# Optimization experiments

Measured on AMD Instinct MI355X. Metric: run time of the kernel, lower is better.

Reference implementation:

```python
import jax, jax.numpy as jnp
import numpy as np

N = 100000   # nodes
C = 128      # in_channels
K = 32       # n_super_nodes
B = 64       # graphs (num segments)


def setup_inputs() -> dict:
    key = jax.random.key(0)
    k_x, k_b, k_w1, k_b1, k_w2, k_b2 = jax.random.split(key, 6)
    x = jax.random.normal(k_x, (N, C), dtype=jnp.float32)
    batch = jnp.sort(jax.random.randint(k_b, (N,), 0, B))
    # assign_mlp params: Linear(C,C) -> ReLU -> Linear(C,K); stored as [in,out]
    W1 = jax.random.normal(k_w1, (C, C), dtype=jnp.float32) / np.sqrt(C)
    b1 = jax.random.normal(k_b1, (C,), dtype=jnp.float32) * 0.01
    W2 = jax.random.normal(k_w2, (C, K), dtype=jnp.float32) / np.sqrt(C)
    b2 = jax.random.normal(k_b2, (K,), dtype=jnp.float32) * 0.01
    return {"x": x, "batch": batch, "W1": W1, "b1": b1, "W2": W2, "b2": b2}


def reference(x, batch, W1, b1, W2, b2):
    # assignment logits: MLP over node features
    h = jax.nn.relu(x @ W1 + b1)          # [N, C]
    s = jax.nn.softmax(h @ W2 + b2, axis=-1)  # [N, K]
    # outer product per node, then scatter-sum by graph id
    x_expanded = x[:, None, :] * s[:, :, None]  # [N, K, C]
    out = jax.ops.segment_sum(x_expanded, batch, num_segments=B)  # [B, K, C]
    return (out, s)
```

## Files before the change

### kernel.cpp

```cpp
#include <hip/hip_runtime.h>
#include <hip/hip_bf16.h>

#define NN 100000
#define CC 128
#define KK 32
#define BB 64
#define CH 4
#define NCHUNK (NN / 32)

typedef __bf16 bf16x8 __attribute__((ext_vector_type(8)));
typedef float  f32x4  __attribute__((ext_vector_type(4)));

__device__ __forceinline__ unsigned short f2bf(float v) {
    union { __bf16 h; unsigned short s; } u;
    u.h = (__bf16)v;
    return u.s;
}
__device__ __forceinline__ float bf2f(unsigned short h) {
    union { unsigned u; float f; } a; a.u = ((unsigned)h) << 16;
    return a.f;
}
__device__ __forceinline__ void unpack_hilo(uint4 a, uint4 b,
                                            bf16x8& hi8, bf16x8& lo8) {
    union { unsigned u[4]; bf16x8 v; } H, L;
    H.u[0] = __builtin_amdgcn_perm(a.y, a.x, 0x05040100u);
    H.u[1] = __builtin_amdgcn_perm(a.w, a.z, 0x05040100u);
    H.u[2] = __builtin_amdgcn_perm(b.y, b.x, 0x05040100u);
    H.u[3] = __builtin_amdgcn_perm(b.w, b.z, 0x05040100u);
    L.u[0] = __builtin_amdgcn_perm(a.y, a.x, 0x07060302u);
    L.u[1] = __builtin_amdgcn_perm(a.w, a.z, 0x07060302u);
    L.u[2] = __builtin_amdgcn_perm(b.y, b.x, 0x07060302u);
    L.u[3] = __builtin_amdgcn_perm(b.w, b.z, 0x07060302u);
    hi8 = H.v; lo8 = L.v;
}

__device__ __forceinline__ void atomAddF(float* p, float v) {
#if defined(__gfx950__) || defined(__gfx942__) || defined(__gfx90a__)
    unsafeAtomicAdd(p, v);
#else
    atomicAdd(p, v);
#endif
}

__global__ __launch_bounds__(256) void hp_prep(const float* __restrict__ W1,
                                               const float* __restrict__ W2,
                                               unsigned short* __restrict__ w1f,
                                               unsigned short* __restrict__ w2f,
                                               float* __restrict__ out_zero) {
    const int t = blockIdx.x * 256 + threadIdx.x;
    {
        const int idx  = t;
        const int j    = idx & 7;
        const int lane = (idx >> 3) & 63;
        const int nt   = (idx >> 9) & 7;
        const int kt   = idx >> 12;
        const int k = kt * 32 + (lane >> 4) * 8 + j;
        const int n = nt * 16 + (lane & 15);
        const float w = W1[k * CC + n];
        const unsigned short h = f2bf(w);
        w1f[idx]         = h;
        w1f[16384 + idx] = f2bf(w - bf2f(h));
    }
    if (t < 4096) {
        const int idx  = t;
        const int j    = idx & 7;
        const int lane = (idx >> 3) & 63;
        const int nt   = (idx >> 9) & 1;
        const int kt   = idx >> 10;
        const int k = kt * 32 + (lane >> 4) * 8 + j;
        const int n = nt * 16 + (lane & 15);
        const float w = W2[k * KK + n];
        const unsigned short h = f2bf(w);
        w2f[idx]        = h;
        w2f[4096 + idx] = f2bf(w - bf2f(h));
    }
    const float4 z = make_float4(0.f, 0.f, 0.f, 0.f);
    for (int i = t; i < BB * KK * CC / 4; i += 16384)
        *(float4*)(out_zero + (size_t)i * 4) = z;
}

__global__ __launch_bounds__(256, 3) void hp_fused(
    const float* __restrict__ x,
    const unsigned short* __restrict__ w1f,
    const unsigned short* __restrict__ w2f,
    const float* __restrict__ b1,
    const float* __restrict__ b2,
    const int* __restrict__ batch,
    float* __restrict__ s_out,
    float* __restrict__ out)
{
    __shared__ __align__(16) char uni[16896];
    __shared__ __align__(16) unsigned short xbL[8 * 64 * 8];
    __shared__ float lgT[32][36];
    __shared__ float redm[4][32];
    __shared__ float reds[4][32];

    unsigned short* xa   = (unsigned short*)uni;
    unsigned int*   hs16 = (unsigned int*)uni;

    const int t    = threadIdx.x;
    const int wave = __builtin_amdgcn_readfirstlane(t >> 6);
    const int lane = t & 63;

    const int pmt   = wave & 1;
    const int chalf = wave >> 1;
    const int nrow  = (lane >> 4) * 8;

    f32x4 pacc[4];
    #pragma unroll
    for (int i = 0; i < 4; ++i) pacc[i] = (f32x4){0.f, 0.f, 0.f, 0.f};

    int cg = __builtin_amdgcn_readfirstlane(batch[blockIdx.x * (CH * 32)]);

    auto flush = [&](int g) {
        float* op = out + (size_t)g * KK * CC;
        #pragma unroll
        for (int i = 0; i < 4; ++i) {
            const int c = (chalf * 4 + i) * 16 + (lane & 15);
            #pragma unroll
            for (int r = 0; r < 4; ++r) {
                const int k = pmt * 16 + (lane >> 4) * 4 + r;
                atomAddF(op + k * CC + c, pacc[i][r]);
            }
            pacc[i] = (f32x4){0.f, 0.f, 0.f, 0.f};
        }
    };

    #pragma unroll 1
    for (int ch = 0; ch < CH; ++ch) {
        const int chunk = blockIdx.x * CH + ch;
        if (chunk >= NCHUNK) break;
        const int base = chunk * 32;

        __syncthreads();

        #pragma unroll
        for (int mt = 0; mt < 2; ++mt) {
            const int q  = mt * 4 + wave;
            const int n  = base + mt * 16 + (lane & 15);
            const int ck = wave * 32 + (lane >> 4) * 8;
            const float4 va = *(const float4*)(x + (size_t)n * CC + ck);
            const float4 vb = *(const float4*)(x + (size_t)n * CC + ck + 4);
            const float v[8] = {va.x, va.y, va.z, va.w, vb.x, vb.y, vb.z, vb.w};
            union { unsigned short s[8]; uint4 u; } H, L;
            #pragma unroll
            for (int j = 0; j < 8; ++j) {
                H.s[j] = f2bf(v[j]);
                L.s[j] = f2bf(v[j] - bf2f(H.s[j]));
            }
            unsigned short* d0 = xa + (q * 64 + lane) * 8;
            *(uint4*)(d0)        = H.u;
            *(uint4*)(d0 + 4096) = L.u;
        }

        #pragma unroll
        for (int cc = 0; cc < 2; ++cc) {
            const int ct = wave * 2 + cc;
            const int c  = ct * 16 + (lane & 15);
            const int nb = base + nrow;
            union { unsigned short s[8]; uint4 u; } Hb;
            #pragma unroll
            for (int j = 0; j < 8; ++j)
                Hb.s[j] = f2bf(x[(size_t)(nb + j) * CC + c]);
            *(uint4*)(xbL + ((size_t)ct * 64 + lane) * 8) = Hb.u;
        }
        __syncthreads();

        f32x4 acc[2][2];
        #pragma unroll
        for (int mt = 0; mt < 2; ++mt)
            #pragma unroll
            for (int nl = 0; nl < 2; ++nl)
                acc[mt][nl] = (f32x4){0.f, 0.f, 0.f, 0.f};

        #pragma unroll
        for (int kt = 0; kt < 4; ++kt) {
            bf16x8 ah[2], al[2];
            #pragma unroll
            for (int mt = 0; mt < 2; ++mt) {
                ah[mt] = *(const bf16x8*)(xa + ((mt * 4 + kt) * 64 + lane) * 8);
                al[mt] = *(const bf16x8*)(xa + 4096 + ((mt * 4 + kt) * 64 + lane) * 8);
            }
            #pragma unroll
            for (int nl = 0; nl < 2; ++nl) {
                const int nt = 2 * wave + nl;
                const bf16x8 wh = *(const bf16x8*)(w1f + ((kt * 8 + nt) * 64 + lane) * 8);
                const bf16x8 wl = *(const bf16x8*)(w1f + 16384 + ((kt * 8 + nt) * 64 + lane) * 8);
                #pragma unroll
                for (int mt = 0; mt < 2; ++mt) {
                    acc[mt][nl] = __builtin_amdgcn_mfma_f32_16x16x32_bf16(ah[mt], wh, acc[mt][nl], 0, 0, 0);
                    acc[mt][nl] = __builtin_amdgcn_mfma_f32_16x16x32_bf16(al[mt], wh, acc[mt][nl], 0, 0, 0);
                    acc[mt][nl] = __builtin_amdgcn_mfma_f32_16x16x32_bf16(ah[mt], wl, acc[mt][nl], 0, 0, 0);
                }
            }
        }
        __syncthreads();

        #pragma unroll
        for (int nl = 0; nl < 2; ++nl) {
            const int c = (2 * wave + nl) * 16 + (lane & 15);
            const float bv = b1[c];
            #pragma unroll
            for (int mt = 0; mt < 2; ++mt)
                #pragma unroll
                for (int r = 0; r < 4; ++r) {
                    const int node = mt * 16 + (lane >> 4) * 4 + r;
                    const float h = fmaxf(acc[mt][nl][r] + bv, 0.f);
                    const unsigned short hi = f2bf(h);
                    const unsigned short lo = f2bf(h - bf2f(hi));
                    hs16[node * 132 + c] = (unsigned)hi | ((unsigned)lo << 16);
                }
        }
        __syncthreads();

        {
            const int mt2 = wave & 1, nt2 = wave >> 1;
            f32x4 dacc = (f32x4){0.f, 0.f, 0.f, 0.f};
            #pragma unroll
            for (int kt = 0; kt < 4; ++kt) {
                const unsigned* hp = hs16 + (mt2 * 16 + (lane & 15)) * 132
                                          + kt * 32 + (lane >> 4) * 8;
                const uint4 u0 = *(const uint4*)hp;
                const uint4 u1 = *(const uint4*)(hp + 4);
                bf16x8 ah, al;
                unpack_hilo(u0, u1, ah, al);
                const bf16x8 wh = *(const bf16x8*)(w2f + ((kt * 2 + nt2) * 64 + lane) * 8);
                const bf16x8 wl = *(const bf16x8*)(w2f + 4096 + ((kt * 2 + nt2) * 64 + lane) * 8);
                dacc = __builtin_amdgcn_mfma_f32_16x16x32_bf16(ah, wh, dacc, 0, 0, 0);
                dacc = __builtin_amdgcn_mfma_f32_16x16x32_bf16(al, wh, dacc, 0, 0, 0);
                dacc = __builtin_amdgcn_mfma_f32_16x16x32_bf16(ah, wl, dacc, 0, 0, 0);
            }
            const int kcol = nt2 * 16 + (lane & 15);
            #pragma unroll
            for (int r = 0; r < 4; ++r) {
                const int node = mt2 * 16 + (lane >> 4) * 4 + r;
                lgT[node][kcol] = dacc[r];
            }
        }
        __syncthreads();

        {
            const int node = lane & 31;
            const int koff = ((lane >> 5) << 4) + wave * 4;
            const float4 bv2 = *(const float4*)(b2 + koff);
            const float4 lv  = *(const float4*)&lgT[node][koff];
            float lg[4] = {lv.x + bv2.x, lv.y + bv2.y, lv.z + bv2.z, lv.w + bv2.w};

            float m = fmaxf(fmaxf(lg[0], lg[1]), fmaxf(lg[2], lg[3]));
            m = fmaxf(m, __shfl_xor(m, 32));
            if (lane < 32) redm[wave][lane] = m;
            __syncthreads();
            const float M = fmaxf(fmaxf(redm[0][node], redm[1][node]),
                                  fmaxf(redm[2][node], redm[3][node]));
            const float e0 = __expf(lg[0] - M);
            const float e1 = __expf(lg[1] - M);
            const float e2 = __expf(lg[2] - M);
            const float e3 = __expf(lg[3] - M);
            float sp = (e0 + e1) + (e2 + e3);
            sp += __shfl_xor(sp, 32);
            if (lane < 32) reds[wave][lane] = sp;
            __syncthreads();
            const float S = (reds[0][node] + reds[1][node]) + (reds[2][node] + reds[3][node]);
            const float inv = 1.f / S;
            const float4 s4 = make_float4(e0 * inv, e1 * inv, e2 * inv, e3 * inv);
            *(float4*)(s_out + (size_t)(base + node) * KK + koff) = s4;
            *(float4*)&lgT[node][koff] = s4;
        }
        __syncthreads();

        {
            union { unsigned short s[8]; bf16x8 v; } A;
            const int kA = pmt * 16 + (lane & 15);
            #pragma unroll
            for (int j = 0; j < 8; ++j)
                A.s[j] = f2bf(lgT[nrow + j][kA]);
            bf16x8 Bv[4];
            #pragma unroll
            for (int i = 0; i < 4; ++i)
                Bv[i] = *(const bf16x8*)(xbL + ((size_t)(chalf * 4 + i) * 64 + lane) * 8);

            const int gl0 = __builtin_amdgcn_readfirstlane(batch[base]);
            const int gh  = __builtin_amdgcn_readfirstlane(batch[base + 31]);

            if (gl0 == cg && gh == cg) {
                #pragma unroll
                for (int i = 0; i < 4; ++i)
                    pacc[i] = __builtin_amdgcn_mfma_f32_16x16x32_bf16(A.v, Bv[i], pacc[i], 0, 0, 0);
            } else {
                int bt[8];
                #pragma unroll
                for (int j = 0; j < 8; ++j) bt[j] = batch[base + nrow + j];
                while (cg < gh) {
                    union { unsigned short s[8]; bf16x8 v; } Am;
                    #pragma unroll
                    for (int j = 0; j < 8; ++j)
                        Am.s[j] = (bt[j] == cg) ? A.s[j] : (unsigned short)0;
                    #pragma unroll
                    for (int i = 0; i < 4; ++i)
                        pacc[i] = __builtin_amdgcn_mfma_f32_16x16x32_bf16(Am.v, Bv[i], pacc[i], 0, 0, 0);
                    flush(cg);
                    ++cg;
                }
                union { unsigned short s[8]; bf16x8 v; } Am;
                #pragma unroll
                for (int j = 0; j < 8; ++j)
                    Am.s[j] = (bt[j] == cg) ? A.s[j] : (unsigned short)0;
                #pragma unroll
                for (int i = 0; i < 4; ++i)
                    pacc[i] = __builtin_amdgcn_mfma_f32_16x16x32_bf16(Am.v, Bv[i], pacc[i], 0, 0, 0);
            }
        }
    }

    flush(cg);
}

extern "C" void kernel_launch(void* const* d_in, const int* in_sizes, int n_in,
                              void* d_out, int out_size, void* d_ws, size_t ws_size,
                              hipStream_t stream) {
    const float* x     = (const float*)d_in[0];
    const int*   batch = (const int*)d_in[1];
    const float* W1    = (const float*)d_in[2];
    const float* b1    = (const float*)d_in[3];
    const float* W2    = (const float*)d_in[4];
    const float* b2    = (const float*)d_in[5];

    float* out = (float*)d_out;
    float* s   = out + (size_t)BB * KK * CC;

    char* ws = (char*)d_ws;
    unsigned short* w1f = (unsigned short*)ws;
    unsigned short* w2f = (unsigned short*)(ws + 65536);

    hp_prep<<<64, 256, 0, stream>>>(W1, W2, w1f, w2f, out);
    const int nblk = (NCHUNK + CH - 1) / CH;
    hp_fused<<<nblk, 256, 0, stream>>>(x, w1f, w2f, b1, b2, batch, s, out);
}
```

Baseline: 132.9 us.

## Fuse logits softmax into MFMA waves and overlap xbL staging with idle waves

Waves 0-1 now compute both 16-column logit tiles and run the softmax in registers with intra-row shuffles. This removes the lgT round-trip, the cross-wave redm/reds reductions and several block barriers. Waves 2-3 stage the bf16 transposed x tile for the pooling MFMA in parallel, and the loop-head barrier is dropped. Bias loads are hoisted out of the loop and launch bounds go from 3 to 4 blocks per CU, which may raise register pressure or cause spills. The s_out stores become scalar strided instead of float4, and the removed loop-top barrier may risk an xbL reuse hazard across chunks.

After: 149.5 us. +12.5%, slower.

```diff
diff --git a/kernel.cpp b/kernel.cpp
--- a/kernel.cpp
+++ b/kernel.cpp
@@ -79,7 +79,7 @@
         *(float4*)(out_zero + (size_t)i * 4) = z;
 }
 
-__global__ __launch_bounds__(256, 3) void hp_fused(
+__global__ __launch_bounds__(256, 4) void hp_fused(
     const float* __restrict__ x,
     const unsigned short* __restrict__ w1f,
     const unsigned short* __restrict__ w2f,
@@ -92,8 +92,6 @@
     __shared__ __align__(16) char uni[16896];
     __shared__ __align__(16) unsigned short xbL[8 * 64 * 8];
     __shared__ float lgT[32][36];
-    __shared__ float redm[4][32];
-    __shared__ float reds[4][32];
 
     unsigned short* xa   = (unsigned short*)uni;
     unsigned int*   hs16 = (unsigned int*)uni;
@@ -105,6 +103,11 @@
     const int pmt   = wave & 1;
     const int chalf = wave >> 1;
     const int nrow  = (lane >> 4) * 8;
+
+    const float bv_epi0 = b1[(2 * wave + 0) * 16 + (lane & 15)];
+    const float bv_epi1 = b1[(2 * wave + 1) * 16 + (lane & 15)];
+    const float b2lo = b2[lane & 15];
+    const float b2hi = b2[16 + (lane & 15)];
 
     f32x4 pacc[4];
     #pragma unroll
@@ -131,8 +134,6 @@
         const int chunk = blockIdx.x * CH + ch;
         if (chunk >= NCHUNK) break;
         const int base = chunk * 32;
-
-        __syncthreads();
 
         #pragma unroll
         for (int mt = 0; mt < 2; ++mt) {
@@ -152,18 +153,6 @@
             *(uint4*)(d0)        = H.u;
             *(uint4*)(d0 + 4096) = L.u;
         }
-
-        #pragma unroll
-        for (int cc = 0; cc < 2; ++cc) {
-            const int ct = wave * 2 + cc;
-            const int c  = ct * 16 + (lane & 15);
-            const int nb = base + nrow;
-            union { unsigned short s[8]; uint4 u; } Hb;
-            #pragma unroll
-            for (int j = 0; j < 8; ++j)
-                Hb.s[j] = f2bf(x[(size_t)(nb + j) * CC + c]);
-            *(uint4*)(xbL + ((size_t)ct * 64 + lane) * 8) = Hb.u;
-        }
         __syncthreads();
 
         f32x4 acc[2][2];
@@ -198,8 +187,8 @@
 
         #pragma unroll
         for (int nl = 0; nl < 2; ++nl) {
+            const float bv = nl ? bv_epi1 : bv_epi0;
             const int c = (2 * wave + nl) * 16 + (lane & 15);
-            const float bv = b1[c];
             #pragma unroll
             for (int mt = 0; mt < 2; ++mt)
                 #pragma unroll
@@ -213,9 +202,11 @@
         }
         __syncthreads();
 
-        {
-            const int mt2 = wave & 1, nt2 = wave >> 1;
-            f32x4 dacc = (f32x4){0.f, 0.f, 0.f, 0.f};
+        if (wave < 2) {
+            const int mt2 = wave;
+            f32x4 dacc[2];
+            dacc[0] = (f32x4){0.f, 0.f, 0.f, 0.f};
+            dacc[1] = (f32x4){0.f, 0.f, 0.f, 0.f};
             #pragma unroll
             for (int kt = 0; kt < 4; ++kt) {
                 const unsigned* hp = hs16 + (mt2 * 16 + (lane & 15)) * 132
@@ -224,47 +215,62 @@
                 const uint4 u1 = *(const uint4*)(hp + 4);
                 bf16x8 ah, al;
                 unpack_hilo(u0, u1, ah, al);
-                const bf16x8 wh = *(const bf16x8*)(w2f + ((kt * 2 + nt2) * 64 + lane) * 8);
-                const bf16x8 wl = *(const bf16x8*)(w2f + 4096 + ((kt * 2 + nt2) * 64 + lane) * 8);
-                dacc = __builtin_amdgcn_mfma_f32_16x16x32_bf16(ah, wh, dacc, 0, 0, 0);
-                dacc = __builtin_amdgcn_mfma_f32_16x16x32_bf16(al, wh, dacc, 0, 0, 0);
-                dacc = __builtin_amdgcn_mfma_f32_16x16x32_bf16(ah, wl, dacc, 0, 0, 0);
-            }
-            const int kcol = nt2 * 16 + (lane & 15);
+                #pragma unroll
+                for (int nt2 = 0; nt2 < 2; ++nt2) {
+                    const bf16x8 wh = *(const bf16x8*)(w2f + ((kt * 2 + nt2) * 64 + lane) * 8);
+                    const bf16x8 wl = *(const bf16x8*)(w2f + 4096 + ((kt * 2 + nt2) * 64 + lane) * 8);
+                    dacc[nt2] = __builtin_amdgcn_mfma_f32_16x16x32_bf16(ah, wh, dacc[nt2], 0, 0, 0);
+                    dacc[nt2] = __builtin_amdgcn_mfma_f32_16x16x32_bf16(al, wh, dacc[nt2], 0, 0, 0);
+                    dacc[nt2] = __builtin_amdgcn_mfma_f32_16x16x32_bf16(ah, wl, dacc[nt2], 0, 0, 0);
+                }
+            }
+            float lg0[4], lg1[4], m[4];
             #pragma unroll
             for (int r = 0; r < 4; ++r) {
+                lg0[r] = dacc[0][r] + b2lo;
+                lg1[r] = dacc[1][r] + b2hi;
+                m[r] = fmaxf(lg0[r], lg1[r]);
+            }
+            #pragma unroll
+            for (int msk = 1; msk < 16; msk <<= 1)
+                #pragma unroll
+                for (int r = 0; r < 4; ++r)
+                    m[r] = fmaxf(m[r], __shfl_xor(m[r], msk));
+            float e0[4], e1[4], sm[4];
+            #pragma unroll
+            for (int r = 0; r < 4; ++r) {
+                e0[r] = __expf(lg0[r] - m[r]);
+                e1[r] = __expf(lg1[r] - m[r]);
+                sm[r] = e0[r] + e1[r];
+            }
+            #pragma unroll
+            for (int msk = 1; msk < 16; msk <<= 1)
+                #pragma unroll
+                for (int r = 0; r < 4; ++r)
+                    sm[r] += __shfl_xor(sm[r], msk);
+            #pragma unroll
+            for (int r = 0; r < 4; ++r) {
+                const float inv = 1.f / sm[r];
+                e0[r] *= inv;
+                e1[r] *= inv;
                 const int node = mt2 * 16 + (lane >> 4) * 4 + r;
-                lgT[node][kcol] = dacc[r];
-            }
-        }
-        __syncthreads();
-
-        {
-            const int node = lane & 31;
-            const int koff = ((lane >> 5) << 4) + wave * 4;
-            const float4 bv2 = *(const float4*)(b2 + koff);
-            const float4 lv  = *(const float4*)&lgT[node][koff];
-            float lg[4] = {lv.x + bv2.x, lv.y + bv2.y, lv.z + bv2.z, lv.w + bv2.w};
-
-            float m = fmaxf(fmaxf(lg[0], lg[1]), fmaxf(lg[2], lg[3]));
-            m = fmaxf(m, __shfl_xor(m, 32));
-            if (lane < 32) redm[wave][lane] = m;
-            __syncthreads();
-            const float M = fmaxf(fmaxf(redm[0][node], redm[1][node]),
-                                  fmaxf(redm[2][node], redm[3][node]));
-            const float e0 = __expf(lg[0] - M);
-            const float e1 = __expf(lg[1] - M);
-            const float e2 = __expf(lg[2] - M);
-            const float e3 = __expf(lg[3] - M);
-            float sp = (e0 + e1) + (e2 + e3);
-            sp += __shfl_xor(sp, 32);
-            if (lane < 32) reds[wave][lane] = sp;
-            __syncthreads();
-            const float S = (reds[0][node] + reds[1][node]) + (reds[2][node] + reds[3][node]);
-            const float inv = 1.f / S;
-            const float4 s4 = make_float4(e0 * inv, e1 * inv, e2 * inv, e3 * inv);
-            *(float4*)(s_out + (size_t)(base + node) * KK + koff) = s4;
-            *(float4*)&lgT[node][koff] = s4;
+                s_out[(size_t)(base + node) * KK + (lane & 15)]      = e0[r];
+                s_out[(size_t)(base + node) * KK + 16 + (lane & 15)] = e1[r];
+                lgT[node][lane & 15]        = e0[r];
+                lgT[node][16 + (lane & 15)] = e1[r];
+            }
+        } else {
+            const int nb = base + nrow;
+            #pragma unroll
+            for (int cc = 0; cc < 4; ++cc) {
+                const int ct = (wave - 2) * 4 + cc;
+                const int c  = ct * 16 + (lane & 15);
+                union { unsigned short s[8]; uint4 u; } Hb;
+                #pragma unroll
+                for (int j = 0; j < 8; ++j)
+                    Hb.s[j] = f2bf(x[(size_t)(nb + j) * CC + c]);
+                *(uint4*)(xbL + ((size_t)ct * 64 + lane) * 8) = Hb.u;
+            }
         }
         __syncthreads();
 
```

## Replace global float atomics with per-block partial slots and a reduction kernel

Applied to the files above, without the earlier changes.

Instead of atomically adding each block's per-graph accumulators into the output, each block writes plain stores into a private slot. The slot index comes from the graph's start node, found by a binary search over the sorted batch array in the prep kernel. A new kernel then sums the 16 slots per graph into the output. This removes atomic contention on shared output addresses, but adds a 16 MB partial buffer that must be zeroed and re-read each call, plus an extra launch. It also assumes no graph spans more than 16 blocks.

Result: slower. 149.0 us (+12.1%).

```diff
diff --git a/kernel.cpp b/kernel.cpp
--- a/kernel.cpp
+++ b/kernel.cpp
@@ -7,6 +7,7 @@
 #define BB 64
 #define CH 4
 #define NCHUNK (NN / 32)
+#define NSLOT 16
 
 typedef __bf16 bf16x8 __attribute__((ext_vector_type(8)));
 typedef float  f32x4  __attribute__((ext_vector_type(4)));
@@ -34,21 +35,24 @@
     hi8 = H.v; lo8 = L.v;
 }
 
-__device__ __forceinline__ void atomAddF(float* p, float v) {
-#if defined(__gfx950__) || defined(__gfx942__) || defined(__gfx90a__)
-    unsafeAtomicAdd(p, v);
-#else
-    atomicAdd(p, v);
-#endif
-}
-
-__global__ __launch_bounds__(256) void hp_prep(const float* __restrict__ W1,
+__global__ __launch_bounds__(256) void hp_prep(const int* __restrict__ batch,
+                                               const float* __restrict__ W1,
                                                const float* __restrict__ W2,
+                                               int* __restrict__ bounds,
                                                unsigned short* __restrict__ w1f,
                                                unsigned short* __restrict__ w2f,
-                                               float* __restrict__ out_zero) {
+                                               float* __restrict__ part) {
+    if (blockIdx.x == 0 && threadIdx.x <= BB) {
+        const int b = threadIdx.x;
+        int lo = 0, hi = NN;
+        while (lo < hi) {
+            const int mid = (lo + hi) >> 1;
+            if (batch[mid] < b) lo = mid + 1; else hi = mid;
+        }
+        bounds[b] = lo;
+    }
     const int t = blockIdx.x * 256 + threadIdx.x;
-    {
+    if (t < 16384) {
         const int idx  = t;
         const int j    = idx & 7;
         const int lane = (idx >> 3) & 63;
@@ -75,8 +79,8 @@
         w2f[4096 + idx] = f2bf(w - bf2f(h));
     }
     const float4 z = make_float4(0.f, 0.f, 0.f, 0.f);
-    for (int i = t; i < BB * KK * CC / 4; i += 16384)
-        *(float4*)(out_zero + (size_t)i * 4) = z;
+    for (int i = t; i < BB * NSLOT * KK * CC / 4; i += 65536)
+        *(float4*)(part + (size_t)i * 4) = z;
 }
 
 __global__ __launch_bounds__(256, 3) void hp_fused(
@@ -86,8 +90,9 @@
     const float* __restrict__ b1,
     const float* __restrict__ b2,
     const int* __restrict__ batch,
+    const int* __restrict__ bounds,
     float* __restrict__ s_out,
-    float* __restrict__ out)
+    float* __restrict__ part)
 {
     __shared__ __align__(16) char uni[16896];
     __shared__ __align__(16) unsigned short xbL[8 * 64 * 8];
@@ -113,14 +118,15 @@
     int cg = __builtin_amdgcn_readfirstlane(batch[blockIdx.x * (CH * 32)]);
 
     auto flush = [&](int g) {
-        float* op = out + (size_t)g * KK * CC;
+        const int slot = blockIdx.x - (bounds[g] >> 7);
+        float* op = part + ((size_t)g * NSLOT + slot) * (KK * CC);
         #pragma unroll
         for (int i = 0; i < 4; ++i) {
             const int c = (chalf * 4 + i) * 16 + (lane & 15);
             #pragma unroll
             for (int r = 0; r < 4; ++r) {
                 const int k = pmt * 16 + (lane >> 4) * 4 + r;
-                atomAddF(op + k * CC + c, pacc[i][r]);
+                op[k * CC + c] = pacc[i][r];
             }
             pacc[i] = (f32x4){0.f, 0.f, 0.f, 0.f};
         }
@@ -315,6 +321,23 @@
     flush(cg);
 }
 
+__global__ __launch_bounds__(256) void hp_reduce(const float* __restrict__ part,
+                                                 float* __restrict__ out) {
+    const int i = (blockIdx.x * 256 + threadIdx.x) * 4;
+    if (i < BB * KK * CC) {
+        const int b = i >> 12;
+        const int j = i & 4095;
+        const float* pp = part + (size_t)b * NSLOT * 4096 + j;
+        float4 r = make_float4(0.f, 0.f, 0.f, 0.f);
+        #pragma unroll 4
+        for (int q = 0; q < NSLOT; ++q) {
+            const float4 v = *(const float4*)(pp + (size_t)q * 4096);
+            r.x += v.x; r.y += v.y; r.z += v.z; r.w += v.w;
+        }
+        *(float4*)(out + i) = r;
+    }
+}
+
 extern "C" void kernel_launch(void* const* d_in, const int* in_sizes, int n_in,
                               void* d_out, int out_size, void* d_ws, size_t ws_size,
                               hipStream_t stream) {
@@ -329,10 +352,13 @@
     float* s   = out + (size_t)BB * KK * CC;
 
     char* ws = (char*)d_ws;
-    unsigned short* w1f = (unsigned short*)ws;
-    unsigned short* w2f = (unsigned short*)(ws + 65536);
-
-    hp_prep<<<64, 256, 0, stream>>>(W1, W2, w1f, w2f, out);
+    int*            bounds = (int*)ws;
+    unsigned short* w1f    = (unsigned short*)(ws + 1024);
+    unsigned short* w2f    = (unsigned short*)(ws + 66560);
+    float*          part   = (float*)(ws + 82944);
+
+    hp_prep<<<256, 256, 0, stream>>>(batch, W1, W2, bounds, w1f, w2f, part);
     const int nblk = (NCHUNK + CH - 1) / CH;
-    hp_fused<<<nblk, 256, 0, stream>>>(x, w1f, w2f, b1, b2, batch, s, out);
-}
+    hp_fused<<<nblk, 256, 0, stream>>>(x, w1f, w2f, b1, b2, batch, bounds, s, part);
+    hp_reduce<<<BB * KK * CC / (256 * 4), 256, 0, stream>>>(part, out);
+}
```
